# Performance work log

Hardware: AMD Instinct MI355X
Metric: run time of the kernel (lower is better)

## Reference

```python
import jax, jax.numpy as jnp
import numpy as np

GROUP_SIZE = 128
SCALE_MIN = 1e-8
IN_FEATURES = 4096
OUT_FEATURES = 4096
BATCH, SEQ = 4, 2048


def quantize_literati(weight, scales):
    """w -> sign(w) * clamp(scale) per group of GROUP_SIZE along last dim.
    in_features is divisible by GROUP_SIZE, so no padding branch is needed.
    """
    O, C = weight.shape
    wg = weight.reshape(O, C // GROUP_SIZE, GROUP_SIZE)
    # torch.sign with zeros mapped to +1
    signs = jnp.where(wg >= 0, 1.0, -1.0).astype(weight.dtype)
    s = jnp.maximum(scales, SCALE_MIN)  # (O, num_groups)
    w_q = signs * s[..., None]
    return w_q.reshape(O, C)


def setup_inputs() -> dict:
    key = jax.random.key(0)
    kx, kw = jax.random.split(key)
    x = jax.random.normal(kx, (BATCH, SEQ, IN_FEATURES), dtype=jnp.float32)
    # kaiming_uniform_(a=sqrt(5)) -> U(-1/sqrt(fan_in), 1/sqrt(fan_in))
    bound = 1.0 / np.sqrt(IN_FEATURES)
    weight = jax.random.uniform(kw, (OUT_FEATURES, IN_FEATURES), dtype=jnp.float32,
                                minval=-bound, maxval=bound)
    scales = jnp.full((OUT_FEATURES, IN_FEATURES // GROUP_SIZE), 0.1, dtype=jnp.float32)
    return {"x": x, "weight": weight, "scales": scales}


def reference(x, weight, scales):
    w_q = quantize_literati(weight, scales)
    # F.linear: x @ w_q.T
    return jnp.einsum('bsc,oc->bso', x, w_q)
```

## Files before the change

### kernel.cpp

```cpp
#include <hip/hip_runtime.h>
#include <hip/hip_bf16.h>
#include <stdint.h>
#include <stddef.h>


#define M_DIM 8192
#define N_DIM 4096
#define K_DIM 4096
#define BM 256
#define BN 256
#define BK 32
#define NT (K_DIM / BK)

typedef __bf16 bf16x8 __attribute__((ext_vector_type(8)));
typedef float f32x4 __attribute__((ext_vector_type(4)));

__device__ __forceinline__ void async_copy16(const void* g, void* l) {
  __builtin_amdgcn_global_load_lds((__attribute__((address_space(1))) void*)g,
                                   (__attribute__((address_space(3))) void*)l,
                                   16, 0, 0);
}

#define X_THREADS ((size_t)M_DIM * K_DIM / 16)
#define W_THREADS ((size_t)N_DIM * K_DIM / 16)
__global__ __launch_bounds__(256) void prep_kernel(
    const float* __restrict__ x, const float* __restrict__ w,
    const float* __restrict__ scales, __bf16* __restrict__ xb,
    __bf16* __restrict__ wb) {
  const size_t t = (size_t)blockIdx.x * blockDim.x + threadIdx.x;
  if (t < X_THREADS) {
    const float4* src = (const float4*)x + t * 4;
    bf16x8* dst = (bf16x8*)xb + t * 2;
#pragma unroll
    for (int h = 0; h < 2; ++h) {
      const float4 v0 = src[h * 2 + 0];
      const float4 v1 = src[h * 2 + 1];
      bf16x8 o;
      o[0] = (__bf16)v0.x; o[1] = (__bf16)v0.y;
      o[2] = (__bf16)v0.z; o[3] = (__bf16)v0.w;
      o[4] = (__bf16)v1.x; o[5] = (__bf16)v1.y;
      o[6] = (__bf16)v1.z; o[7] = (__bf16)v1.w;
      dst[h] = o;
    }
  } else {
    const size_t u = t - X_THREADS;
    const size_t idx = u * 16;
    const int o_ = (int)(idx >> 12);
    const int grp = (int)(idx & 4095) >> 7;
    const float s = fmaxf(scales[(o_ << 5) + grp], 1e-8f);
    const float4* src = (const float4*)w + u * 4;
    bf16x8* dst = (bf16x8*)wb + u * 2;
#pragma unroll
    for (int h = 0; h < 2; ++h) {
      const float4 v0 = src[h * 2 + 0];
      const float4 v1 = src[h * 2 + 1];
      bf16x8 q;
      q[0] = (__bf16)((v0.x >= 0.f) ? s : -s);
      q[1] = (__bf16)((v0.y >= 0.f) ? s : -s);
      q[2] = (__bf16)((v0.z >= 0.f) ? s : -s);
      q[3] = (__bf16)((v0.w >= 0.f) ? s : -s);
      q[4] = (__bf16)((v1.x >= 0.f) ? s : -s);
      q[5] = (__bf16)((v1.y >= 0.f) ? s : -s);
      q[6] = (__bf16)((v1.z >= 0.f) ? s : -s);
      q[7] = (__bf16)((v1.w >= 0.f) ? s : -s);
      dst[h] = q;
    }
  }
}


#define LDS_A(b) ((char*)lds + (b) * 32768)
#define LDS_B(b) ((char*)lds + (b) * 32768 + 16384)

#define STAGE_A(tt) do {                                              \
    char* _d = LDS_A((tt) & 3);                                       \
    async_copy16(aS[0] + (size_t)(tt) * BK, _d + dOff[0]);            \
    async_copy16(aS[1] + (size_t)(tt) * BK, _d + dOff[1]);            \
  } while (0)

#define STAGE_B(tt) do {                                              \
    char* _d = LDS_B((tt) & 3);                                       \
    async_copy16(bS[0] + (size_t)(tt) * BK, _d + dOff[0]);            \
    async_copy16(bS[1] + (size_t)(tt) * BK, _d + dOff[1]);            \
  } while (0)

#define TILE_BODY(tt, DO_STAGE, VMSTR) do {                                    \
    char* _bufA = LDS_A((tt) & 3);                                             \
    char* _bufB = LDS_B((tt) & 3);                                             \
    bf16x8 _av[4]; bf16x8 _bv[4];                                              \
                                             \
    _Pragma("unroll") for (int _i = 0; _i < 4; ++_i)                           \
      _av[_i] = *(const bf16x8*)(_bufA + aOff[0][_i]);                         \
    _Pragma("unroll") for (int _j = 0; _j < 4; ++_j)                           \
      _bv[_j] = *(const bf16x8*)(_bufB + bOff[_j]);                            \
    if (DO_STAGE) STAGE_A((tt) + 3);                                           \
    __builtin_amdgcn_s_barrier();                                              \
    asm volatile("s_waitcnt lgkmcnt(0)" ::: "memory");                         \
    __builtin_amdgcn_sched_barrier(0);                                         \
    __builtin_amdgcn_s_setprio(1);                                             \
    _Pragma("unroll") for (int _i = 0; _i < 4; ++_i)                           \
      _Pragma("unroll") for (int _j = 0; _j < 4; ++_j)                         \
        acc[_i][_j] = __builtin_amdgcn_mfma_f32_16x16x32_bf16(                 \
            _av[_i], _bv[_j], acc[_i][_j], 0, 0, 0);                           \
    __builtin_amdgcn_s_setprio(0);                                             \
    __builtin_amdgcn_s_barrier();                                              \
                             \
    _Pragma("unroll") for (int _i = 0; _i < 4; ++_i)                           \
      _av[_i] = *(const bf16x8*)(_bufA + aOff[1][_i]);                         \
    if (DO_STAGE) STAGE_B((tt) + 3);                                           \
    __builtin_amdgcn_s_barrier();                                              \
    asm volatile("s_waitcnt lgkmcnt(0)" ::: "memory");                         \
    __builtin_amdgcn_sched_barrier(0);                                         \
    __builtin_amdgcn_s_setprio(1);                                             \
    _Pragma("unroll") for (int _i = 0; _i < 4; ++_i)                           \
      _Pragma("unroll") for (int _j = 0; _j < 4; ++_j)                         \
        acc[4 + _i][_j] = __builtin_amdgcn_mfma_f32_16x16x32_bf16(             \
            _av[_i], _bv[_j], acc[4 + _i][_j], 0, 0, 0);                       \
    __builtin_amdgcn_s_setprio(0);                                             \
    asm volatile("s_waitcnt " VMSTR ::: "memory");                             \
    __builtin_amdgcn_s_barrier();                                              \
  } while (0)

__global__ __launch_bounds__(512, 2) void literati_gemm(
    const __bf16* __restrict__ Ab, const __bf16* __restrict__ Bb,
    float* __restrict__ C) {
  __shared__ __align__(16) char lds[4 * 32768];

  const int tid = threadIdx.x;
  const int lane = tid & 63;
  const int wave = tid >> 6;
  const int bn0 = blockIdx.x * BN;
  const int bm0 = blockIdx.y * BM;
  const int wm = wave >> 2;
  const int wn = wave & 3;

  const int r_in = lane >> 2;
  const int kc_st = (lane & 3) ^ ((lane >> 3) & 3);
  const __bf16* aS[2];
  const __bf16* bS[2];
  int dOff[2];
#pragma unroll
  for (int i = 0; i < 2; ++i) {
    const int c64 = wave * 2 + i;
    aS[i] = Ab + (size_t)(bm0 + c64 * 16 + r_in) * K_DIM + kc_st * 8;
    bS[i] = Bb + (size_t)(bn0 + c64 * 16 + r_in) * K_DIM + kc_st * 8;
    dOff[i] = (c64 * 64 + lane) * 16;
  }

  const int fr = lane & 15;
  const int kc_rd = lane >> 4;
  int aOff[2][4], bOff[4];
#pragma unroll
  for (int mh = 0; mh < 2; ++mh)
#pragma unroll
    for (int i = 0; i < 4; ++i) {
      const int row = wm * 128 + mh * 64 + i * 16 + fr;
      aOff[mh][i] = (row * 4 + (kc_rd ^ ((row >> 1) & 3))) * 16;
    }
#pragma unroll
  for (int j = 0; j < 4; ++j) {
    const int row = wn * 64 + j * 16 + fr;
    bOff[j] = (row * 4 + (kc_rd ^ ((row >> 1) & 3))) * 16;
  }

  f32x4 acc[8][4];
#pragma unroll
  for (int f = 0; f < 8; ++f)
#pragma unroll
    for (int j = 0; j < 4; ++j)
#pragma unroll
      for (int r = 0; r < 4; ++r) acc[f][j][r] = 0.f;

#pragma unroll
  for (int tt = 0; tt < 3; ++tt) {
    STAGE_A(tt);
    STAGE_B(tt);
  }
  asm volatile("s_waitcnt vmcnt(8)" ::: "memory");
  __builtin_amdgcn_s_barrier();

  for (int t = 0; t < NT - 3; ++t) TILE_BODY(t, 1, "vmcnt(8)");
  TILE_BODY(NT - 3, 0, "vmcnt(4)");
  TILE_BODY(NT - 2, 0, "vmcnt(0)");
  TILE_BODY(NT - 1, 0, "vmcnt(0)");

  const int col0 = bn0 + wn * 64 + fr;
  const int rbase = bm0 + wm * 128 + (lane >> 4) * 4;
#pragma unroll
  for (int mh = 0; mh < 2; ++mh)
#pragma unroll
    for (int i = 0; i < 4; ++i) {
      const int row0 = rbase + mh * 64 + i * 16;
#pragma unroll
      for (int j = 0; j < 4; ++j) {
        float* p = C + (size_t)row0 * N_DIM + col0 + j * 16;
#pragma unroll
        for (int r = 0; r < 4; ++r)
          p[(size_t)r * N_DIM] = acc[mh * 4 + i][j][r];
      }
    }
}

extern "C" void kernel_launch(void* const* d_in, const int* in_sizes, int n_in,
                              void* d_out, int out_size, void* d_ws, size_t ws_size,
                              hipStream_t stream) {
  (void)in_sizes; (void)n_in; (void)out_size;
  const float* x = (const float*)d_in[0];
  const float* w = (const float*)d_in[1];
  const float* sc = (const float*)d_in[2];
  float* out = (float*)d_out;

  __bf16* xb = (__bf16*)d_ws;
  __bf16* wb = xb + (size_t)M_DIM * K_DIM;
  (void)ws_size;

  const size_t total_threads = X_THREADS + W_THREADS;
  prep_kernel<<<(int)(total_threads / 256), 256, 0, stream>>>(x, w, sc, xb, wb);

  dim3 grid(N_DIM / BN, M_DIM / BM);
  literati_gemm<<<grid, 512, 0, stream>>>(xb, wb, out);
}
```

Measured before the change: 493.7 us.

## Unroll GEMM main loop by four and prefetch both A fragment halves

The GEMM K-loop is unrolled by four, so each LDS ring buffer index is a compile-time constant. Global source pointers are now bumped incrementally instead of recomputed from the tile index. Both halves of the A fragments are read from LDS before the first MFMA block, and the explicit lgkmcnt(0) waits and mid-tile sched_barriers are removed so the compiler can overlap LDS reads with MFMAs. This trims address arithmetic and the second LDS-read stall per tile, at the cost of more live VGPRs and less manual control over instruction ordering.

```diff
diff --git a/kernel.cpp b/kernel.cpp
--- a/kernel.cpp
+++ b/kernel.cpp
@@ -72,53 +72,51 @@
 #define LDS_A(b) ((char*)lds + (b) * 32768)
 #define LDS_B(b) ((char*)lds + (b) * 32768 + 16384)
 
-#define STAGE_A(tt) do {                                              \
-    char* _d = LDS_A((tt) & 3);                                       \
-    async_copy16(aS[0] + (size_t)(tt) * BK, _d + dOff[0]);            \
-    async_copy16(aS[1] + (size_t)(tt) * BK, _d + dOff[1]);            \
+#define STAGE_A_TO(b) do {                        \
+    char* _d = LDS_A(b);                          \
+    async_copy16(aP0, _d + dO0);                  \
+    async_copy16(aP1, _d + dO1);                  \
   } while (0)
 
-#define STAGE_B(tt) do {                                              \
-    char* _d = LDS_B((tt) & 3);                                       \
-    async_copy16(bS[0] + (size_t)(tt) * BK, _d + dOff[0]);            \
-    async_copy16(bS[1] + (size_t)(tt) * BK, _d + dOff[1]);            \
+#define STAGE_B_TO(b) do {                        \
+    char* _d = LDS_B(b);                          \
+    async_copy16(bP0, _d + dO0);                  \
+    async_copy16(bP1, _d + dO1);                  \
   } while (0)
 
-#define TILE_BODY(tt, DO_STAGE, VMSTR) do {                                    \
-    char* _bufA = LDS_A((tt) & 3);                                             \
-    char* _bufB = LDS_B((tt) & 3);                                             \
-    bf16x8 _av[4]; bf16x8 _bv[4];                                              \
-                                             \
-    _Pragma("unroll") for (int _i = 0; _i < 4; ++_i)                           \
-      _av[_i] = *(const bf16x8*)(_bufA + aOff[0][_i]);                         \
+#define ADVANCE do { aP0 += BK; aP1 += BK; bP0 += BK; bP1 += BK; } while (0)
+
+#define TILE_BODY(BUF, DO_STAGE, VMSTR) do {                                   \
+    char* _bufA = LDS_A(BUF);                                                  \
+    char* _bufB = LDS_B(BUF);                                                  \
+    bf16x8 _av0[4], _av1[4], _bv[4];                                           \
+       \
+    _Pragma("unroll") for (int _i = 0; _i < 4; ++_i)                           \
+      _av0[_i] = *(const bf16x8*)(_bufA + aOff[0][_i]);                        \
     _Pragma("unroll") for (int _j = 0; _j < 4; ++_j)                           \
       _bv[_j] = *(const bf16x8*)(_bufB + bOff[_j]);                            \
-    if (DO_STAGE) STAGE_A((tt) + 3);                                           \
-    __builtin_amdgcn_s_barrier();                                              \
-    asm volatile("s_waitcnt lgkmcnt(0)" ::: "memory");                         \
-    __builtin_amdgcn_sched_barrier(0);                                         \
+    _Pragma("unroll") for (int _i = 0; _i < 4; ++_i)                           \
+      _av1[_i] = *(const bf16x8*)(_bufA + aOff[1][_i]);                        \
+    if (DO_STAGE) STAGE_A_TO((BUF + 3) & 3);                                   \
+    __builtin_amdgcn_s_barrier();                                              \
     __builtin_amdgcn_s_setprio(1);                                             \
     _Pragma("unroll") for (int _i = 0; _i < 4; ++_i)                           \
       _Pragma("unroll") for (int _j = 0; _j < 4; ++_j)                         \
         acc[_i][_j] = __builtin_amdgcn_mfma_f32_16x16x32_bf16(                 \
-            _av[_i], _bv[_j], acc[_i][_j], 0, 0, 0);                           \
+            _av0[_i], _bv[_j], acc[_i][_j], 0, 0, 0);                          \
     __builtin_amdgcn_s_setprio(0);                                             \
     __builtin_amdgcn_s_barrier();                                              \
-                             \
-    _Pragma("unroll") for (int _i = 0; _i < 4; ++_i)                           \
-      _av[_i] = *(const bf16x8*)(_bufA + aOff[1][_i]);                         \
-    if (DO_STAGE) STAGE_B((tt) + 3);                                           \
-    __builtin_amdgcn_s_barrier();                                              \
-    asm volatile("s_waitcnt lgkmcnt(0)" ::: "memory");                         \
-    __builtin_amdgcn_sched_barrier(0);                                         \
+    if (DO_STAGE) { STAGE_B_TO((BUF + 3) & 3); ADVANCE; }                      \
+    __builtin_amdgcn_s_barrier();                                              \
     __builtin_amdgcn_s_setprio(1);                                             \
     _Pragma("unroll") for (int _i = 0; _i < 4; ++_i)                           \
       _Pragma("unroll") for (int _j = 0; _j < 4; ++_j)                         \
         acc[4 + _i][_j] = __builtin_amdgcn_mfma_f32_16x16x32_bf16(             \
-            _av[_i], _bv[_j], acc[4 + _i][_j], 0, 0, 0);                       \
+            _av1[_i], _bv[_j], acc[4 + _i][_j], 0, 0, 0);                      \
     __builtin_amdgcn_s_setprio(0);                                             \
     asm volatile("s_waitcnt " VMSTR ::: "memory");                             \
     __builtin_amdgcn_s_barrier();                                              \
+    __builtin_amdgcn_sched_barrier(0);    \
   } while (0)
 
 __global__ __launch_bounds__(512, 2) void literati_gemm(
@@ -136,16 +134,13 @@
 
   const int r_in = lane >> 2;
   const int kc_st = (lane & 3) ^ ((lane >> 3) & 3);
-  const __bf16* aS[2];
-  const __bf16* bS[2];
-  int dOff[2];
-#pragma unroll
-  for (int i = 0; i < 2; ++i) {
-    const int c64 = wave * 2 + i;
-    aS[i] = Ab + (size_t)(bm0 + c64 * 16 + r_in) * K_DIM + kc_st * 8;
-    bS[i] = Bb + (size_t)(bn0 + c64 * 16 + r_in) * K_DIM + kc_st * 8;
-    dOff[i] = (c64 * 64 + lane) * 16;
-  }
+  const int c0 = wave * 2;
+  const __bf16* aP0 = Ab + (size_t)(bm0 + c0 * 16 + r_in) * K_DIM + kc_st * 8;
+  const __bf16* aP1 = Ab + (size_t)(bm0 + (c0 + 1) * 16 + r_in) * K_DIM + kc_st * 8;
+  const __bf16* bP0 = Bb + (size_t)(bn0 + c0 * 16 + r_in) * K_DIM + kc_st * 8;
+  const __bf16* bP1 = Bb + (size_t)(bn0 + (c0 + 1) * 16 + r_in) * K_DIM + kc_st * 8;
+  const int dO0 = (c0 * 64 + lane) * 16;
+  const int dO1 = ((c0 + 1) * 64 + lane) * 16;
 
   const int fr = lane & 15;
   const int kc_rd = lane >> 4;
@@ -171,18 +166,23 @@
 #pragma unroll
       for (int r = 0; r < 4; ++r) acc[f][j][r] = 0.f;
 
-#pragma unroll
-  for (int tt = 0; tt < 3; ++tt) {
-    STAGE_A(tt);
-    STAGE_B(tt);
-  }
+  STAGE_A_TO(0); STAGE_B_TO(0); ADVANCE;
+  STAGE_A_TO(1); STAGE_B_TO(1); ADVANCE;
+  STAGE_A_TO(2); STAGE_B_TO(2); ADVANCE;
   asm volatile("s_waitcnt vmcnt(8)" ::: "memory");
   __builtin_amdgcn_s_barrier();
-
-  for (int t = 0; t < NT - 3; ++t) TILE_BODY(t, 1, "vmcnt(8)");
-  TILE_BODY(NT - 3, 0, "vmcnt(4)");
-  TILE_BODY(NT - 2, 0, "vmcnt(0)");
-  TILE_BODY(NT - 1, 0, "vmcnt(0)");
+  __builtin_amdgcn_sched_barrier(0);
+
+  for (int tq = 0; tq < 31; ++tq) {
+    TILE_BODY(0, 1, "vmcnt(8)");
+    TILE_BODY(1, 1, "vmcnt(8)");
+    TILE_BODY(2, 1, "vmcnt(8)");
+    TILE_BODY(3, 1, "vmcnt(8)");
+  }
+  TILE_BODY(0, 1, "vmcnt(8)");
+  TILE_BODY(1, 0, "vmcnt(4)");
+  TILE_BODY(2, 0, "vmcnt(0)");
+  TILE_BODY(3, 0, "vmcnt(0)");
 
   const int col0 = bn0 + wn * 64 + fr;
   const int rbase = bm0 + wm * 128 + (lane >> 4) * 4;
@@ -204,7 +204,7 @@
 extern "C" void kernel_launch(void* const* d_in, const int* in_sizes, int n_in,
                               void* d_out, int out_size, void* d_ws, size_t ws_size,
                               hipStream_t stream) {
-  (void)in_sizes; (void)n_in; (void)out_size;
+  (void)in_sizes; (void)n_in; (void)out_size; (void)ws_size;
   const float* x = (const float*)d_in[0];
   const float* w = (const float*)d_in[1];
   const float* sc = (const float*)d_in[2];
@@ -212,7 +212,6 @@
 
   __bf16* xb = (__bf16*)d_ws;
   __bf16* wb = xb + (size_t)M_DIM * K_DIM;
-  (void)ws_size;
 
   const size_t total_threads = X_THREADS + W_THREADS;
   prep_kernel<<<(int)(total_threads / 256), 256, 0, stream>>>(x, w, sc, xb, wb);
```

New measurement: 486.2 us. Within noise of the previous version (-1.5%).
